# Performance work log

Hardware: AMD Instinct MI355X
Metric: run time of the kernel (lower is better)

Reference implementation:

```python
import jax, jax.numpy as jnp
import numpy as np

# ---- module hyperparameters (init_kwargs) ----
QMIN, QMAX, QBINS = -8.0, 8.0, 128
PMIN, PMAX, PBINS = -10.0, 10.0, 128
GAMMA_F = 1.0
N_TRAJ = 16384


def _grid():
    # x = arange(qmin - 4/gamma_f, qmax + 4/gamma_f + 0.1/maxp, 0.1/maxp)
    maxp = max(abs(PMIN), abs(PMAX))
    step = 0.1 / maxp
    x = np.arange(QMIN - 4.0 / GAMMA_F, QMAX + 4.0 / GAMMA_F + step, step)
    return x.astype(np.float32)


def setup_inputs() -> dict:
    key = jax.random.key(0)
    ks = jax.random.split(key, 6)
    shape = (1, N_TRAJ)
    x = jnp.asarray(_grid())
    # psi buffer: stand-in for np.interp(x, spl.x, spl.psis[-1][1]) -- a
    # localized oscillatory wavefunction sampled on the grid.
    psi = (jnp.exp(-0.5 * (x - 1.0) ** 2) * jnp.cos(2.0 * x)).astype(jnp.float32)
    return {
        "factors_re": jax.random.normal(ks[0], shape, jnp.float32),
        "factors_im": jax.random.normal(ks[1], shape, jnp.float32),
        "q_re": jax.random.normal(ks[2], shape, jnp.float32),
        "q_im": 0.5 * jax.random.normal(ks[3], shape, jnp.float32),
        "p_re": jax.random.normal(ks[4], shape, jnp.float32),
        "p_im": 0.5 * jax.random.normal(ks[5], shape, jnp.float32),
        "x": x,
        "psi": psi,
    }


def _trapz0(y, x):
    # trapezoid rule along axis 0; y: [M, N] (complex), x: [M]
    dx = jnp.diff(x)
    return jnp.sum(0.5 * (y[1:] + y[:-1]) * dx[:, None], axis=0)


def _forward(factors_re, factors_im, q_re, q_im, p_re, p_im, x, psi):
    g = GAMMA_F
    factors = factors_re + 1j * factors_im  # [1, N] complex
    # _calc_proj: xi = 2*g*q + 1j*p ; qf = Re(xi)/(2g), pf = Im(xi)
    qf = q_re - p_im / (2.0 * g)
    pf = 2.0 * g * q_im + p_re
    dq = (QMAX - QMIN) / QBINS
    dp = (PMAX - PMIN) / PBINS
    qb = jnp.floor((qf - QMIN) / dq)
    pb = jnp.floor((pf - PMIN) / dp)
    bins = (qb * PBINS + pb).astype(jnp.int32).reshape(-1)  # [N]
    n = bins.shape[0]
    # torch: enumerate(torch.unique(bins)) -> rank among sorted unique values.
    # jnp.unique inverse (size=n, large fill pads at the end) gives the same map.
    _, inv = jnp.unique(bins, return_inverse=True, size=n, fill_value=jnp.int32(2**30))
    inds = inv.reshape(qf.shape)  # [1, N] compact bin ids
    qc = (qb + 0.5) * dq + QMIN  # bin centers [1, N]
    pc = (pb + 0.5) * dp + PMIN
    # _gf: coherent-state Gaussians on grid x -> [M, N]
    norm = (2.0 * g / jnp.pi) ** 0.25
    dxq = x[:, None] - qc.reshape(-1)[None, :]  # [M, N]
    gfs = norm * jnp.exp(-g * dxq * dxq + 1j * pc.reshape(-1)[None, :] * dxq)
    gt = _trapz0(jnp.conj(gfs) * psi[:, None], x)  # [N] complex
    # _calc_pref (reconstruction): exponential prefactor that can blow up,
    # hence the nan_to_num + clamp in the original.
    pref = norm * jnp.exp(g * q_im * q_im + 1j * (p_re * q_im))  # [1, N]
    pref = (jnp.clip(jnp.nan_to_num(pref.real), -100.0, 100.0)
            + 1j * jnp.clip(jnp.nan_to_num(pref.imag), -100.0, 100.0))
    vals = pref * factors  # [1, N]
    b = vals.shape[0]
    binned = jnp.zeros_like(vals).at[jnp.arange(b)[:, None], inds].add(vals)
    loss = jnp.sum(jnp.abs(binned - gt[None, :]) ** 2)
    return jnp.sqrt(loss)


def reference(factors_re, factors_im, q_re, q_im, p_re, p_im, x, psi):
    return _forward(factors_re, factors_im, q_re, q_im, p_re, p_im, x, psi)
```

## Files before the change

kernel.cpp:

```cpp
#include <hip/hip_runtime.h>
#include <math.h>


#define PRES_WORDS 1024
#define PRES_BITS  65536
#define PRES_OFF   32768
#define CHUNKS     16
#define MCAP       2432
#define WINR       4.0f
#define NORM       0.8932438417380023f

__global__ void __launch_bounds__(256) gt_kernel(
    const float* __restrict__ q_re, const float* __restrict__ q_im,
    const float* __restrict__ p_re, const float* __restrict__ p_im,
    const float* __restrict__ x, const float* __restrict__ psi,
    unsigned long long* __restrict__ pres,
    float* __restrict__ bre, float* __restrict__ bim,
    float* __restrict__ gpre, float* __restrict__ gpim, int n, int M)
{
    __shared__ float swpsi[MCAP];
    int tid = threadIdx.x;
    float x0 = x[0];
    float h  = x[1] - x0;
    for (int m = tid; m < M; m += 256) {
        float w = (m == 0 || m == M - 1) ? 0.5f * h : h;
        swpsi[m] = w * psi[m] * NORM;
    }
    __syncthreads();
    int t = blockIdx.x * 256 + tid;
    if (t >= n) return;
    float qi = q_im[t], pr = p_re[t];
    float qf = q_re[t] - 0.5f * p_im[t];
    float pf = 2.0f * qi + pr;
    float qb = floorf((qf - (-8.0f)) / 0.125f);
    float pb = floorf((pf - (-10.0f)) / 0.15625f);
    float qcn = (qb + 0.5f) * 0.125f + (-8.0f);
    float pcn = (pb + 0.5f) * 0.15625f + (-10.0f);
    if (blockIdx.y == 0) {
        int b = (int)(qb * 128.0f + pb);
        int pidx = min(max(b + PRES_OFF, 0), PRES_BITS - 1);
        atomicOr(&pres[pidx >> 6], 1ull << (pidx & 63));
        bre[t] = 0.0f; bim[t] = 0.0f;
    }
    float inv_h = 1.0f / h;
    int mlo = max(0, (int)((qcn - WINR - x0) * inv_h) - 1);
    int mhi = min(M, (int)((qcn + WINR - x0) * inv_h) + 2);
    int len = mhi - mlo; if (len < 0) len = 0;
    int c = blockIdx.y;
    int ms = mlo + (len * c) / CHUNKS;
    int me = mlo + (len * (c + 1)) / CHUNKS;
    float b0  = x0 - qcn;
    float dx0 = fmaf((float)ms, h, b0);
    float e   = __expf(-dx0 * dx0);
    float u   = __expf(-h * (dx0 + dx0 + h));
    float d   = __expf(-2.0f * h * h);
    float sn, cs, sd, cd;
    __sincosf(pcn * dx0, &sn, &cs);
    __sincosf(pcn * h, &sd, &cd);
    float sre = 0.0f, sim = 0.0f;
    for (int m = ms; m < me; m++) {
        float w = swpsi[m];
        float tv = e * w;
        sre = fmaf(tv, cs, sre);
        sim = fmaf(-tv, sn, sim);
        e *= u; u *= d;
        float cn = fmaf(cs, cd, -sn * sd);
        sn = fmaf(sn, cd, cs * sd);
        cs = cn;
    }
    gpre[c * n + t] = sre;
    gpim[c * n + t] = sim;
}

__global__ void __launch_bounds__(256) scatter_loss_kernel(
    const float* __restrict__ f_re, const float* __restrict__ f_im,
    const float* __restrict__ q_re, const float* __restrict__ q_im,
    const float* __restrict__ p_re, const float* __restrict__ p_im,
    const unsigned long long* __restrict__ pres,
    float* __restrict__ bre, float* __restrict__ bim,
    const float* __restrict__ gpre, const float* __restrict__ gpim,
    int* __restrict__ k3done, float* __restrict__ loss, int* __restrict__ fin,
    float* __restrict__ out, int n)
{
    __shared__ int lbase[PRES_WORDS];
    int tid = threadIdx.x;
    if (tid < 64) {
        int cum[16];
        int tot = 0;
        for (int k = 0; k < 16; k++) { cum[k] = tot; tot += __popcll(pres[tid * 16 + k]); }
        int run = tot;
        for (int off = 1; off < 64; off <<= 1) {
            int up = __shfl_up(run, off);
            if (tid >= off) run += up;
        }
        int excl = run - tot;
        for (int k = 0; k < 16; k++) lbase[tid * 16 + k] = excl + cum[k];
    }
    __syncthreads();
    int t = blockIdx.x * 256 + tid;
    float sre = 0.0f, sim = 0.0f;
    for (int c = 0; c < CHUNKS; c++) {
        sre += gpre[c * n + t];
        sim += gpim[c * n + t];
    }
    float qi = q_im[t], pr = p_re[t];
    float qf = q_re[t] - 0.5f * p_im[t];
    float pf = 2.0f * qi + pr;
    float qb = floorf((qf - (-8.0f)) / 0.125f);
    float pb = floorf((pf - (-10.0f)) / 0.15625f);
    int b = (int)(qb * 128.0f + pb);
    int pidx = min(max(b + PRES_OFF, 0), PRES_BITS - 1);
    int w = pidx >> 6, bit = pidx & 63;
    unsigned long long below = pres[w] & ((bit == 0) ? 0ull : (~0ull >> (64 - bit)));
    int cid = lbase[w] + __popcll(below);
    float ea = NORM * expf(qi * qi);
    float s, c2;
    __sincosf(pr * qi, &s, &c2);
    float prr = fminf(fmaxf(ea * c2, -100.0f), 100.0f);
    float pri = fminf(fmaxf(ea * s, -100.0f), 100.0f);
    float fr = f_re[t], fi = f_im[t];
    atomicAdd(&bre[cid], prr * fr - pri * fi);
    atomicAdd(&bim[cid], prr * fi + pri * fr);
    __threadfence();
    __syncthreads();
    if (tid == 0) {
        __hip_atomic_fetch_add(k3done, 1, __ATOMIC_ACQ_REL, __HIP_MEMORY_SCOPE_AGENT);
        while (__hip_atomic_load(k3done, __ATOMIC_ACQUIRE, __HIP_MEMORY_SCOPE_AGENT)
               < (int)gridDim.x)
            __builtin_amdgcn_s_sleep(4);
    }
    __syncthreads();
    float brt = __hip_atomic_load(&bre[t], __ATOMIC_RELAXED, __HIP_MEMORY_SCOPE_AGENT);
    float bit2 = __hip_atomic_load(&bim[t], __ATOMIC_RELAXED, __HIP_MEMORY_SCOPE_AGENT);
    float dre = brt - sre;
    float dim = bit2 - sim;
    float v = dre * dre + dim * dim;
#pragma unroll
    for (int off = 32; off > 0; off >>= 1) v += __shfl_down(v, off);
    __shared__ float l[4];
    int wv = tid >> 6, ln = tid & 63;
    if (ln == 0) l[wv] = v;
    __syncthreads();
    if (tid == 0) {
        __hip_atomic_fetch_add(loss, l[0] + l[1] + l[2] + l[3],
                               __ATOMIC_ACQ_REL, __HIP_MEMORY_SCOPE_AGENT);
        int old = __hip_atomic_fetch_add(fin, 1, __ATOMIC_ACQ_REL,
                                         __HIP_MEMORY_SCOPE_AGENT);
        if (old == (int)gridDim.x - 1) {
            out[0] = sqrtf(__hip_atomic_load(loss, __ATOMIC_ACQUIRE,
                                             __HIP_MEMORY_SCOPE_AGENT));
        }
    }
}

extern "C" void kernel_launch(void* const* d_in, const int* in_sizes, int n_in,
                              void* d_out, int out_size, void* d_ws, size_t ws_size,
                              hipStream_t stream)
{
    const float* f_re = (const float*)d_in[0];
    const float* f_im = (const float*)d_in[1];
    const float* q_re = (const float*)d_in[2];
    const float* q_im = (const float*)d_in[3];
    const float* p_re = (const float*)d_in[4];
    const float* p_im = (const float*)d_in[5];
    const float* x    = (const float*)d_in[6];
    const float* psi  = (const float*)d_in[7];
    int n = in_sizes[0];
    int M = in_sizes[6];

    float* gpre = (float*)d_ws;
    float* gpim = gpre + (size_t)CHUNKS * n;
    float* bre  = gpim + (size_t)CHUNKS * n;
    float* bim  = bre + n;
    unsigned long long* pres = (unsigned long long*)(bim + n);
    float* loss    = (float*)(pres + PRES_WORDS);
    int*   k3done  = (int*)(loss + 1);
    int*   fin     = k3done + 1;

    hipMemsetAsync(pres, 0, PRES_WORDS * sizeof(unsigned long long) + 12, stream);

    int nb = (n + 255) / 256;
    gt_kernel<<<dim3(nb, CHUNKS), 256, 0, stream>>>(q_re, q_im, p_re, p_im, x, psi,
                                                    pres, bre, bim, gpre, gpim, n, M);
    scatter_loss_kernel<<<nb, 256, 0, stream>>>(f_re, f_im, q_re, q_im, p_re, p_im,
                                                pres, bre, bim, gpre, gpim,
                                                k3done, loss, fin, (float*)d_out, n);
}
```

Measured before the change: 107.8 us.

## Fuse Gaussian projection and scatter-loss kernels with grid barriers, narrow window

Merges the projection kernel and the scatter/loss kernel into one launch, using an arrival counter so the chunk-0 blocks wait for all partial sums before compacting bins, scattering and reducing. Halves the chunk count so fewer blocks are launched, and shrinks the Gaussian integration window from 4 to 3.5 widths to cut loop iterations. This removes one kernel launch and the gap between the two kernels. The risks are spin-wait deadlock if not all blocks are co-resident, and slightly larger truncation error.

```diff
diff --git a/kernel.cpp b/kernel.cpp
--- a/kernel.cpp
+++ b/kernel.cpp
@@ -5,20 +5,28 @@
 #define PRES_WORDS 1024
 #define PRES_BITS  65536
 #define PRES_OFF   32768
-#define CHUNKS     16
+#define CHUNKS     8
 #define MCAP       2432
-#define WINR       4.0f
+#define WINR       3.5f
 #define NORM       0.8932438417380023f
 
-__global__ void __launch_bounds__(256) gt_kernel(
+#define AL(p) __hip_atomic_load((p), __ATOMIC_RELAXED, __HIP_MEMORY_SCOPE_AGENT)
+
+__global__ void __launch_bounds__(256) fused_kernel(
+    const float* __restrict__ f_re, const float* __restrict__ f_im,
     const float* __restrict__ q_re, const float* __restrict__ q_im,
     const float* __restrict__ p_re, const float* __restrict__ p_im,
     const float* __restrict__ x, const float* __restrict__ psi,
     unsigned long long* __restrict__ pres,
     float* __restrict__ bre, float* __restrict__ bim,
-    float* __restrict__ gpre, float* __restrict__ gpim, int n, int M)
+    float* __restrict__ gpre, float* __restrict__ gpim,
+    int* __restrict__ arrive1, int* __restrict__ arrive2,
+    float* __restrict__ loss, int* __restrict__ fin,
+    float* __restrict__ out, int n, int M)
 {
     __shared__ float swpsi[MCAP];
+    __shared__ int lbase[PRES_WORDS];
+    __shared__ float lred[4];
     int tid = threadIdx.x;
     float x0 = x[0];
     float h  = x[1] - x0;
@@ -27,18 +35,19 @@
         swpsi[m] = w * psi[m] * NORM;
     }
     __syncthreads();
-    int t = blockIdx.x * 256 + tid;
-    if (t >= n) return;
+    int traw = blockIdx.x * 256 + tid;
+    bool valid = traw < n;
+    int t = valid ? traw : (n - 1);
+    int cyc = blockIdx.y;
     float qi = q_im[t], pr = p_re[t];
     float qf = q_re[t] - 0.5f * p_im[t];
     float pf = 2.0f * qi + pr;
-    float qb = floorf((qf - (-8.0f)) / 0.125f);
-    float pb = floorf((pf - (-10.0f)) / 0.15625f);
-    float qcn = (qb + 0.5f) * 0.125f + (-8.0f);
-    float pcn = (pb + 0.5f) * 0.15625f + (-10.0f);
-    if (blockIdx.y == 0) {
-        int b = (int)(qb * 128.0f + pb);
-        int pidx = min(max(b + PRES_OFF, 0), PRES_BITS - 1);
+    float qb = floorf((qf + 8.0f) / 0.125f);
+    float pb = floorf((pf + 10.0f) / 0.15625f);
+    float qcn = (qb + 0.5f) * 0.125f - 8.0f;
+    float pcn = (pb + 0.5f) * 0.15625f - 10.0f;
+    int pidx = min(max((int)(qb * 128.0f + pb) + PRES_OFF, 0), PRES_BITS - 1);
+    if (cyc == 0 && valid) {
         atomicOr(&pres[pidx >> 6], 1ull << (pidx & 63));
         bre[t] = 0.0f; bim[t] = 0.0f;
     }
@@ -46,14 +55,12 @@
     int mlo = max(0, (int)((qcn - WINR - x0) * inv_h) - 1);
     int mhi = min(M, (int)((qcn + WINR - x0) * inv_h) + 2);
     int len = mhi - mlo; if (len < 0) len = 0;
-    int c = blockIdx.y;
-    int ms = mlo + (len * c) / CHUNKS;
-    int me = mlo + (len * (c + 1)) / CHUNKS;
-    float b0  = x0 - qcn;
-    float dx0 = fmaf((float)ms, h, b0);
-    float e   = __expf(-dx0 * dx0);
-    float u   = __expf(-h * (dx0 + dx0 + h));
-    float d   = __expf(-2.0f * h * h);
+    int ms = mlo + (len * cyc) / CHUNKS;
+    int me = mlo + (len * (cyc + 1)) / CHUNKS;
+    float dx0 = fmaf((float)ms, h, x0 - qcn);
+    float e = __expf(-dx0 * dx0);
+    float u = __expf(-h * (dx0 + dx0 + h));
+    float d = __expf(-2.0f * h * h);
     float sn, cs, sd, cd;
     __sincosf(pcn * dx0, &sn, &cs);
     __sincosf(pcn * h, &sd, &cd);
@@ -68,26 +75,26 @@
         sn = fmaf(sn, cd, cs * sd);
         cs = cn;
     }
-    gpre[c * n + t] = sre;
-    gpim[c * n + t] = sim;
-}
-
-__global__ void __launch_bounds__(256) scatter_loss_kernel(
-    const float* __restrict__ f_re, const float* __restrict__ f_im,
-    const float* __restrict__ q_re, const float* __restrict__ q_im,
-    const float* __restrict__ p_re, const float* __restrict__ p_im,
-    const unsigned long long* __restrict__ pres,
-    float* __restrict__ bre, float* __restrict__ bim,
-    const float* __restrict__ gpre, const float* __restrict__ gpim,
-    int* __restrict__ k3done, float* __restrict__ loss, int* __restrict__ fin,
-    float* __restrict__ out, int n)
-{
-    __shared__ int lbase[PRES_WORDS];
-    int tid = threadIdx.x;
+    gpre[cyc * n + t] = sre;
+    gpim[cyc * n + t] = sim;
+    __threadfence();
+    __syncthreads();
+    if (tid == 0)
+        __hip_atomic_fetch_add(arrive1, 1, __ATOMIC_ACQ_REL, __HIP_MEMORY_SCOPE_AGENT);
+    if (cyc != 0) return;
+    if (tid == 0) {
+        int total = (int)(gridDim.x * gridDim.y);
+        while (__hip_atomic_load(arrive1, __ATOMIC_ACQUIRE, __HIP_MEMORY_SCOPE_AGENT) < total)
+            __builtin_amdgcn_s_sleep(2);
+    }
+    __syncthreads();
     if (tid < 64) {
         int cum[16];
         int tot = 0;
-        for (int k = 0; k < 16; k++) { cum[k] = tot; tot += __popcll(pres[tid * 16 + k]); }
+        for (int k = 0; k < 16; k++) {
+            cum[k] = tot;
+            tot += __popcll(AL(&pres[tid * 16 + k]));
+        }
         int run = tot;
         for (int off = 1; off < 64; off <<= 1) {
             int up = __shfl_up(run, off);
@@ -97,59 +104,52 @@
         for (int k = 0; k < 16; k++) lbase[tid * 16 + k] = excl + cum[k];
     }
     __syncthreads();
-    int t = blockIdx.x * 256 + tid;
-    float sre = 0.0f, sim = 0.0f;
-    for (int c = 0; c < CHUNKS; c++) {
-        sre += gpre[c * n + t];
-        sim += gpim[c * n + t];
+    for (int c = 1; c < CHUNKS; c++) {
+        sre += AL(&gpre[c * n + t]);
+        sim += AL(&gpim[c * n + t]);
     }
-    float qi = q_im[t], pr = p_re[t];
-    float qf = q_re[t] - 0.5f * p_im[t];
-    float pf = 2.0f * qi + pr;
-    float qb = floorf((qf - (-8.0f)) / 0.125f);
-    float pb = floorf((pf - (-10.0f)) / 0.15625f);
-    int b = (int)(qb * 128.0f + pb);
-    int pidx = min(max(b + PRES_OFF, 0), PRES_BITS - 1);
-    int w = pidx >> 6, bit = pidx & 63;
-    unsigned long long below = pres[w] & ((bit == 0) ? 0ull : (~0ull >> (64 - bit)));
-    int cid = lbase[w] + __popcll(below);
-    float ea = NORM * expf(qi * qi);
-    float s, c2;
-    __sincosf(pr * qi, &s, &c2);
-    float prr = fminf(fmaxf(ea * c2, -100.0f), 100.0f);
-    float pri = fminf(fmaxf(ea * s, -100.0f), 100.0f);
-    float fr = f_re[t], fi = f_im[t];
-    atomicAdd(&bre[cid], prr * fr - pri * fi);
-    atomicAdd(&bim[cid], prr * fi + pri * fr);
+    if (valid) {
+        unsigned long long pw = AL(&pres[pidx >> 6]);
+        int bit = pidx & 63;
+        unsigned long long below = pw & ((bit == 0) ? 0ull : (~0ull >> (64 - bit)));
+        int cid = lbase[pidx >> 6] + __popcll(below);
+        float ea = NORM * expf(qi * qi);
+        float s2, c2;
+        __sincosf(pr * qi, &s2, &c2);
+        float prr = fminf(fmaxf(ea * c2, -100.0f), 100.0f);
+        float pri = fminf(fmaxf(ea * s2, -100.0f), 100.0f);
+        float fr = f_re[t], fi = f_im[t];
+        atomicAdd(&bre[cid], prr * fr - pri * fi);
+        atomicAdd(&bim[cid], prr * fi + pri * fr);
+    }
     __threadfence();
     __syncthreads();
     if (tid == 0) {
-        __hip_atomic_fetch_add(k3done, 1, __ATOMIC_ACQ_REL, __HIP_MEMORY_SCOPE_AGENT);
-        while (__hip_atomic_load(k3done, __ATOMIC_ACQUIRE, __HIP_MEMORY_SCOPE_AGENT)
+        __hip_atomic_fetch_add(arrive2, 1, __ATOMIC_ACQ_REL, __HIP_MEMORY_SCOPE_AGENT);
+        while (__hip_atomic_load(arrive2, __ATOMIC_ACQUIRE, __HIP_MEMORY_SCOPE_AGENT)
                < (int)gridDim.x)
-            __builtin_amdgcn_s_sleep(4);
+            __builtin_amdgcn_s_sleep(2);
     }
     __syncthreads();
-    float brt = __hip_atomic_load(&bre[t], __ATOMIC_RELAXED, __HIP_MEMORY_SCOPE_AGENT);
-    float bit2 = __hip_atomic_load(&bim[t], __ATOMIC_RELAXED, __HIP_MEMORY_SCOPE_AGENT);
-    float dre = brt - sre;
-    float dim = bit2 - sim;
-    float v = dre * dre + dim * dim;
+    float v = 0.0f;
+    if (valid) {
+        float dre = AL(&bre[t]) - sre;
+        float dim = AL(&bim[t]) - sim;
+        v = dre * dre + dim * dim;
+    }
 #pragma unroll
     for (int off = 32; off > 0; off >>= 1) v += __shfl_down(v, off);
-    __shared__ float l[4];
     int wv = tid >> 6, ln = tid & 63;
-    if (ln == 0) l[wv] = v;
+    if (ln == 0) lred[wv] = v;
     __syncthreads();
     if (tid == 0) {
-        __hip_atomic_fetch_add(loss, l[0] + l[1] + l[2] + l[3],
+        __hip_atomic_fetch_add(loss, lred[0] + lred[1] + lred[2] + lred[3],
                                __ATOMIC_ACQ_REL, __HIP_MEMORY_SCOPE_AGENT);
         int old = __hip_atomic_fetch_add(fin, 1, __ATOMIC_ACQ_REL,
                                          __HIP_MEMORY_SCOPE_AGENT);
-        if (old == (int)gridDim.x - 1) {
+        if (old == (int)gridDim.x - 1)
             out[0] = sqrtf(__hip_atomic_load(loss, __ATOMIC_ACQUIRE,
                                              __HIP_MEMORY_SCOPE_AGENT));
-        }
     }
 }
 
@@ -174,15 +174,15 @@
     float* bim  = bre + n;
     unsigned long long* pres = (unsigned long long*)(bim + n);
     float* loss    = (float*)(pres + PRES_WORDS);
-    int*   k3done  = (int*)(loss + 1);
-    int*   fin     = k3done + 1;
+    int*   arrive1 = (int*)(loss + 1);
+    int*   arrive2 = arrive1 + 1;
+    int*   fin     = arrive2 + 1;
 
-    hipMemsetAsync(pres, 0, PRES_WORDS * sizeof(unsigned long long) + 12, stream);
+    hipMemsetAsync(pres, 0, PRES_WORDS * sizeof(unsigned long long) + 16, stream);
 
     int nb = (n + 255) / 256;
-    gt_kernel<<<dim3(nb, CHUNKS), 256, 0, stream>>>(q_re, q_im, p_re, p_im, x, psi,
-                                                    pres, bre, bim, gpre, gpim, n, M);
-    scatter_loss_kernel<<<nb, 256, 0, stream>>>(f_re, f_im, q_re, q_im, p_re, p_im,
-                                                pres, bre, bim, gpre, gpim,
-                                                k3done, loss, fin, (float*)d_out, n);
+    fused_kernel<<<dim3(nb, CHUNKS), 256, 0, stream>>>(
+        f_re, f_im, q_re, q_im, p_re, p_im, x, psi,
+        pres, bre, bim, gpre, gpim, arrive1, arrive2, loss, fin,
+        (float*)d_out, n, M);
 }
```

Result: slower. 143.8 us (+33.3%).
